# Performance work log

Measured on AMD Instinct MI355X. Metric: run time of the kernel, lower is better.

The kernel has to match this reference:

```python
import jax, jax.numpy as jnp
import numpy as np

H = 16  # num_heads

def setup_inputs() -> dict:
    key = jax.random.key(0)
    ks = jax.random.split(key, 9)
    B, S, D = 4, 1024, 1024
    s = 0.02
    return {
        "x": jax.random.normal(ks[0], (B, S, D), jnp.float32),
        "Wq": jax.random.normal(ks[1], (D, D), jnp.float32) * s,
        "bq": jax.random.normal(ks[2], (D,), jnp.float32) * s,
        "Wk": jax.random.normal(ks[3], (D, D), jnp.float32) * s,
        "bk": jax.random.normal(ks[4], (D,), jnp.float32) * s,
        "Wv": jax.random.normal(ks[5], (D, D), jnp.float32) * s,
        "bv": jax.random.normal(ks[6], (D,), jnp.float32) * s,
        "Wo": jax.random.normal(ks[7], (D, D), jnp.float32) * s,
        "bo": jax.random.normal(ks[8], (D,), jnp.float32) * s,
    }

def reference(x, Wq, bq, Wk, bk, Wv, bv, Wo, bo):
    B, S, D = x.shape
    hd = D // H
    # Batched equivalent of the per-head Linear loop: project then split into heads.
    def proj(W, b):
        return (x @ W + b).reshape(B, S, H, hd).transpose(0, 2, 1, 3)  # [B,H,S,hd]
    q, k, v = proj(Wq, bq), proj(Wk, bk), proj(Wv, bv)
    scores = jnp.einsum("bhqd,bhkd->bhqk", q, k) / jnp.sqrt(jnp.float32(hd))
    probs = jax.nn.softmax(scores, axis=-1)  # [B,H,S,S] (dropout p=0 -> identity)
    ctx = jnp.einsum("bhqk,bhkd->bhqd", probs, v)  # [B,H,S,hd]
    ctx = ctx.transpose(0, 2, 1, 3).reshape(B, S, D)  # concat heads
    out = ctx @ Wo + bo
    return out, probs
```

## Files before the change

kernel.cpp:

```cpp
#include <hip/hip_runtime.h>
#include <math.h>

typedef unsigned short u16;
typedef __attribute__((ext_vector_type(8))) short short8;
typedef __attribute__((ext_vector_type(4))) float f32x4;

#define BB 4
#define SS 1024
#define DD 1024
#define NH 16
#define HD 64
#define BH 64

__device__ __forceinline__ u16 f2bf(float f) {
    union { float f; unsigned u; } v;
    v.f = f;
    unsigned r = v.u + 0x7fffu + ((v.u >> 16) & 1u);
    return (u16)(r >> 16);
}

__device__ __forceinline__ void gll16(const void* g, void* l) {
    __builtin_amdgcn_global_load_lds((__attribute__((address_space(1))) void*)g,
                                     (__attribute__((address_space(3))) void*)l, 16, 0, 0);
}

__global__ void cast_bf16(const float* __restrict__ X, u16* __restrict__ Y) {
    const int i = blockIdx.x * blockDim.x + threadIdx.x;
    const float4 v = reinterpret_cast<const float4*>(X)[i];
    ushort4 o;
    o.x = f2bf(v.x); o.y = f2bf(v.y); o.z = f2bf(v.z); o.w = f2bf(v.w);
    reinterpret_cast<ushort4*>(Y)[i] = o;
}

__global__ void transpose_cast_w(const float* __restrict__ W0, const float* __restrict__ W1,
                                 const float* __restrict__ W2, const float* __restrict__ W3,
                                 u16* __restrict__ O0, u16* __restrict__ O1,
                                 u16* __restrict__ O2, u16* __restrict__ O3) {
    __shared__ float T[64][65];
    const int z = blockIdx.z;
    const float* W = (z == 0) ? W0 : (z == 1) ? W1 : (z == 2) ? W2 : W3;
    u16* O = (z == 0) ? O0 : (z == 1) ? O1 : (z == 2) ? O2 : O3;
    const int k0 = blockIdx.x * 64, n0 = blockIdx.y * 64;
    const int x = threadIdx.x & 63, yq = threadIdx.x >> 6;
#pragma unroll
    for (int r = 0; r < 16; r++) {
        const int row = yq * 16 + r;
        T[row][x] = W[(size_t)(k0 + row) * 1024 + n0 + x];
    }
    __syncthreads();
#pragma unroll
    for (int r = 0; r < 16; r++) {
        const int row = yq * 16 + r;
        O[(size_t)(n0 + row) * 1024 + k0 + x] = f2bf(T[x][row]);
    }
}

__global__ void transpose_v(const u16* __restrict__ V, u16* __restrict__ VT) {
    __shared__ u16 T[64][66];
    const int t0 = blockIdx.x * 64;
    const size_t hbase = (size_t)blockIdx.y * (SS * HD);
    const int x = threadIdx.x & 63, yq = threadIdx.x >> 6;
#pragma unroll
    for (int r = 0; r < 16; r++) {
        const int trow = yq * 16 + r;
        T[trow][x] = V[hbase + (size_t)(t0 + trow) * 64 + x];
    }
    __syncthreads();
#pragma unroll
    for (int r = 0; r < 16; r++) {
        const int drow = yq * 16 + r;
        VT[hbase + (size_t)drow * 1024 + t0 + x] = T[x][drow];
    }
}

template <int MODE, int QKV, int NJC>
__global__ __launch_bounds__(256) void mfma_gemm(
    const u16* __restrict__ A,
    const u16* __restrict__ Bt0, const u16* __restrict__ Bt1, const u16* __restrict__ Bt2,
    const float* __restrict__ bias0, const float* __restrict__ bias1, const float* __restrict__ bias2,
    void* __restrict__ out0, void* __restrict__ out1, void* __restrict__ out2) {
    constexpr int BN = 32 * NJC;
    __shared__ __align__(16) u16 As[128][32];
    __shared__ __align__(16) u16 Bs[BN][32];

    const u16* Bt = Bt0;
    const float* bias = bias0;
    void* out = out0;
    if (QKV) {
        const int z = blockIdx.z;
        Bt = (z == 0) ? Bt0 : (z == 1) ? Bt1 : Bt2;
        bias = (z == 0) ? bias0 : (z == 1) ? bias1 : bias2;
        out = (z == 0) ? out0 : (z == 1) ? out1 : out2;
    }

    const int tid = threadIdx.x;
    const int w = tid >> 6, lane = tid & 63, l15 = lane & 15, quad = lane >> 4;
    const int wr = w >> 1, wc = w & 1;
    const int m0 = blockIdx.y * 128, n0 = blockIdx.x * BN;

    f32x4 acc[4][NJC];
#pragma unroll
    for (int i = 0; i < 4; i++)
#pragma unroll
        for (int j = 0; j < NJC; j++) acc[i][j] = (f32x4){0.f, 0.f, 0.f, 0.f};

    for (int k0 = 0; k0 < 1024; k0 += 32) {
#pragma unroll
        for (int i = 0; i < 2; i++) {
            const int c = i * 256 + tid;
            gll16(A + (size_t)(m0 + (c >> 2)) * 1024 + k0 + (c & 3) * 8,
                  &As[0][0] + (size_t)(i * 256 + (tid & ~63)) * 8);
        }
#pragma unroll
        for (int i = 0; i < BN / 64; i++) {
            const int c = i * 256 + tid;
            gll16(Bt + (size_t)(n0 + (c >> 2)) * 1024 + k0 + (c & 3) * 8,
                  &Bs[0][0] + (size_t)(i * 256 + (tid & ~63)) * 8);
        }
        __syncthreads();
        short8 af[4], bf[NJC];
#pragma unroll
        for (int i = 0; i < 4; i++)
            af[i] = *(const short8*)(&As[wr * 64 + i * 16 + l15][quad * 8]);
#pragma unroll
        for (int j = 0; j < NJC; j++)
            bf[j] = *(const short8*)(&Bs[wc * 16 * NJC + j * 16 + l15][quad * 8]);
#pragma unroll
        for (int i = 0; i < 4; i++)
#pragma unroll
            for (int j = 0; j < NJC; j++)
                acc[i][j] = __builtin_amdgcn_mfma_f32_16x16x32_bf16(af[i], bf[j], acc[i][j], 0, 0, 0);
        __syncthreads();
    }

#pragma unroll
    for (int i = 0; i < 4; i++) {
#pragma unroll
        for (int j = 0; j < NJC; j++) {
            const int nn = n0 + wc * 16 * NJC + j * 16 + l15;
            const float bb = bias[nn];
#pragma unroll
            for (int r = 0; r < 4; r++) {
                const int mm = m0 + wr * 64 + i * 16 + quad * 4 + r;
                const float val = acc[i][j][r] + bb;
                if (MODE == 0) {
                    const int b = mm >> 10, s = mm & 1023, h = nn >> 6, d = nn & 63;
                    ((u16*)out)[((size_t)(b * NH + h) * SS + s) * HD + d] = f2bf(val);
                } else {
                    ((float*)out)[(size_t)mm * 1024 + nn] = val;
                }
            }
        }
    }
}

__global__ __launch_bounds__(256) void attn_fused(
    const u16* __restrict__ Qg, const u16* __restrict__ Kg, const u16* __restrict__ VTg,
    float* __restrict__ probs, u16* __restrict__ ctx) {
    __shared__ __align__(16) u16 Ks[2][2][64][32];
    __shared__ __align__(16) u16 Vs[2][2][64][32];
    __shared__ __align__(16) u16 Ps[4][2][16][32];

    const int tid = threadIdx.x;
    const int w = tid >> 6, lane = tid & 63, l15 = lane & 15, quad = lane >> 4;

    const int bid = blockIdx.y * 16 + blockIdx.x;
    const int work = (bid & 7) * 128 + (bid >> 3);
    const int bh = work >> 4;
    const int s0 = (work & 15) * 64;
    const size_t hbase = (size_t)bh * (SS * HD);

    const int qg = s0 + w * 16 + l15;
    const short8 bq0 = *(const short8*)(Qg + hbase + (size_t)qg * 64 + quad * 8);
    const short8 bq1 = *(const short8*)(Qg + hbase + (size_t)qg * 64 + 32 + quad * 8);

    auto stageK = [&](int buf, int kt) {
#pragma unroll
        for (int i = 0; i < 2; i++) {
            const int c = i * 256 + tid;
            const int ks = c >> 8, row = (c >> 2) & 63, ch = c & 3;
            const int cb = i * 256 + (tid & ~63);
            gll16(Kg + hbase + (size_t)(kt * 64 + row) * 64 + ks * 32 + ch * 8,
                  &Ks[buf][0][0][0] + (size_t)cb * 8);
        }
    };
    auto stageV = [&](int buf, int kt) {
#pragma unroll
        for (int i = 0; i < 2; i++) {
            const int c = i * 256 + tid;
            const int ks = c >> 8, row = (c >> 2) & 63, ch = c & 3;
            const int cb = i * 256 + (tid & ~63);
            gll16(VTg + hbase + (size_t)row * 1024 + kt * 64 + ks * 32 + ch * 8,
                  &Vs[buf][0][0][0] + (size_t)cb * 8);
        }
    };

    float l_i = 0.f;
    stageK(0, 0);
    asm volatile("s_waitcnt vmcnt(0)" ::: "memory");
    __builtin_amdgcn_s_barrier();
#pragma unroll 1
    for (int kt = 0; kt < 16; kt++) {
        const int cur = kt & 1;
        if (kt < 15) stageK(cur ^ 1, kt + 1);
        float ss = 0.f;
#pragma unroll
        for (int c = 0; c < 4; c++) {
            const short8 ak0 = *(const short8*)(&Ks[cur][0][c * 16 + l15][quad * 8]);
            const short8 ak1 = *(const short8*)(&Ks[cur][1][c * 16 + l15][quad * 8]);
            f32x4 z = {0.f, 0.f, 0.f, 0.f};
            z = __builtin_amdgcn_mfma_f32_16x16x32_bf16(ak0, bq0, z, 0, 0, 0);
            z = __builtin_amdgcn_mfma_f32_16x16x32_bf16(ak1, bq1, z, 0, 0, 0);
#pragma unroll
            for (int r = 0; r < 4; r++) ss += __expf(z[r] * 0.125f);
        }
        ss += __shfl_xor(ss, 16);
        ss += __shfl_xor(ss, 32);
        l_i += ss;
        asm volatile("s_waitcnt vmcnt(0)" ::: "memory");
        __builtin_amdgcn_s_barrier();
    }
    const float nlog = -__logf(l_i);

    f32x4 oacc[4];
#pragma unroll
    for (int j = 0; j < 4; j++) oacc[j] = (f32x4){0.f, 0.f, 0.f, 0.f};

    const size_t prow = ((size_t)bh * SS + qg) * SS;

    stageK(0, 0);
    stageV(0, 0);
    asm volatile("s_waitcnt vmcnt(0)" ::: "memory");
    __builtin_amdgcn_s_barrier();

#pragma unroll 1
    for (int kt = 0; kt < 16; kt++) {
        const int cur = kt & 1;
        if (kt < 15) { stageK(cur ^ 1, kt + 1); stageV(cur ^ 1, kt + 1); }

        f32x4 sc[4];
        __builtin_amdgcn_s_setprio(1);
#pragma unroll
        for (int c = 0; c < 4; c++) {
            const short8 ak0 = *(const short8*)(&Ks[cur][0][c * 16 + l15][quad * 8]);
            const short8 ak1 = *(const short8*)(&Ks[cur][1][c * 16 + l15][quad * 8]);
            f32x4 z = {0.f, 0.f, 0.f, 0.f};
            z = __builtin_amdgcn_mfma_f32_16x16x32_bf16(ak0, bq0, z, 0, 0, 0);
            z = __builtin_amdgcn_mfma_f32_16x16x32_bf16(ak1, bq1, z, 0, 0, 0);
            sc[c] = z;
        }
        __builtin_amdgcn_s_setprio(0);
#pragma unroll
        for (int c = 0; c < 4; c++) {
            float p[4];
            f32x4 pv;
#pragma unroll
            for (int r = 0; r < 4; r++) {
                p[r] = __expf(fmaf(sc[c][r], 0.125f, nlog));
                pv[r] = p[r];
            }
            *(f32x4*)(probs + prow + kt * 64 + c * 16 + quad * 4) = pv;
            uint2 pk;
            pk.x = (unsigned)f2bf(p[0]) | ((unsigned)f2bf(p[1]) << 16);
            pk.y = (unsigned)f2bf(p[2]) | ((unsigned)f2bf(p[3]) << 16);
            *(uint2*)(&Ps[w][c >> 1][l15][(c & 1) * 16 + quad * 4]) = pk;
        }
        const short8 ap0 = *(const short8*)(&Ps[w][0][l15][quad * 8]);
        const short8 ap1 = *(const short8*)(&Ps[w][1][l15][quad * 8]);
        __builtin_amdgcn_s_setprio(1);
#pragma unroll
        for (int j = 0; j < 4; j++) {
            const short8 bv0 = *(const short8*)(&Vs[cur][0][j * 16 + l15][quad * 8]);
            const short8 bv1 = *(const short8*)(&Vs[cur][1][j * 16 + l15][quad * 8]);
            oacc[j] = __builtin_amdgcn_mfma_f32_16x16x32_bf16(ap0, bv0, oacc[j], 0, 0, 0);
            oacc[j] = __builtin_amdgcn_mfma_f32_16x16x32_bf16(ap1, bv1, oacc[j], 0, 0, 0);
        }
        __builtin_amdgcn_s_setprio(0);
        asm volatile("s_waitcnt vmcnt(4)" ::: "memory");
        __builtin_amdgcn_s_barrier();
    }

    const int b = bh >> 4, h = bh & 15;
#pragma unroll
    for (int j = 0; j < 4; j++)
#pragma unroll
        for (int r = 0; r < 4; r++) {
            const int s = s0 + w * 16 + quad * 4 + r;
            ctx[((size_t)b * SS + s) * DD + h * HD + j * 16 + l15] = f2bf(oacc[j][r]);
        }
}

extern "C" void kernel_launch(void* const* d_in, const int* in_sizes, int n_in,
                              void* d_out, int out_size, void* d_ws, size_t ws_size,
                              hipStream_t stream) {
    const float* x  = (const float*)d_in[0];
    const float* Wq = (const float*)d_in[1];
    const float* bq = (const float*)d_in[2];
    const float* Wk = (const float*)d_in[3];
    const float* bk = (const float*)d_in[4];
    const float* Wv = (const float*)d_in[5];
    const float* bv = (const float*)d_in[6];
    const float* Wo = (const float*)d_in[7];
    const float* bo = (const float*)d_in[8];

    float* out   = (float*)d_out;
    float* probs = out + (size_t)BB * SS * DD;

    char* ws = (char*)d_ws;
    u16* xb   = (u16*)(ws);
    u16* Wtq  = (u16*)(ws + (8ull << 20));
    u16* Wtk  = (u16*)(ws + (10ull << 20));
    u16* Wtv  = (u16*)(ws + (12ull << 20));
    u16* Wto  = (u16*)(ws + (14ull << 20));
    u16* qb   = (u16*)(ws + (16ull << 20));
    u16* kb   = (u16*)(ws + (24ull << 20));
    u16* vb   = (u16*)(ws + (32ull << 20));
    u16* vTb  = (u16*)(ws + (40ull << 20));
    u16* ctxb = (u16*)(ws + (48ull << 20));

    const dim3 blk(256);

    cast_bf16<<<dim3(4096), blk, 0, stream>>>(x, xb);
    transpose_cast_w<<<dim3(16, 16, 4), blk, 0, stream>>>(Wq, Wk, Wv, Wo, Wtq, Wtk, Wtv, Wto);

    mfma_gemm<0, 1, 4><<<dim3(8, 32, 3), blk, 0, stream>>>(
        xb, Wtq, Wtk, Wtv, bq, bk, bv, qb, kb, vb);

    transpose_v<<<dim3(16, 64), blk, 0, stream>>>(vb, vTb);

    attn_fused<<<dim3(16, 64), blk, 0, stream>>>(qb, kb, vTb, probs, ctxb);

    mfma_gemm<1, 0, 2><<<dim3(16, 32), blk, 0, stream>>>(
        ctxb, Wto, nullptr, nullptr, bo, nullptr, nullptr, out, nullptr, nullptr);
}
```

Measured before the change: 428.6 us.

## Write V transposed from QKV GEMM and double attention block size to 512

The QKV projection GEMM now writes the V output directly in [bh][d][s] transposed layout using 4-wide vector stores, which removes the separate transpose_v kernel and its extra global round trip. The attention kernel moves to 512 threads (8 waves) covering 128 query rows per block, so each staged K/V tile is shared by twice as many query rows and each thread issues one async load per tile instead of two. In exchange, the block uses more LDS and registers, and the grid halves, which may reduce occupancy or load balance.

```diff
diff --git a/kernel.cpp b/kernel.cpp
--- a/kernel.cpp
+++ b/kernel.cpp
@@ -55,24 +55,6 @@
     }
 }
 
-__global__ void transpose_v(const u16* __restrict__ V, u16* __restrict__ VT) {
-    __shared__ u16 T[64][66];
-    const int t0 = blockIdx.x * 64;
-    const size_t hbase = (size_t)blockIdx.y * (SS * HD);
-    const int x = threadIdx.x & 63, yq = threadIdx.x >> 6;
-#pragma unroll
-    for (int r = 0; r < 16; r++) {
-        const int trow = yq * 16 + r;
-        T[trow][x] = V[hbase + (size_t)(t0 + trow) * 64 + x];
-    }
-    __syncthreads();
-#pragma unroll
-    for (int r = 0; r < 16; r++) {
-        const int drow = yq * 16 + r;
-        VT[hbase + (size_t)drow * 1024 + t0 + x] = T[x][drow];
-    }
-}
-
 template <int MODE, int QKV, int NJC>
 __global__ __launch_bounds__(256) void mfma_gemm(
     const u16* __restrict__ A,
@@ -86,11 +68,11 @@
     const u16* Bt = Bt0;
     const float* bias = bias0;
     void* out = out0;
+    const int zz = QKV ? blockIdx.z : 0;
     if (QKV) {
-        const int z = blockIdx.z;
-        Bt = (z == 0) ? Bt0 : (z == 1) ? Bt1 : Bt2;
-        bias = (z == 0) ? bias0 : (z == 1) ? bias1 : bias2;
-        out = (z == 0) ? out0 : (z == 1) ? out1 : out2;
+        Bt = (zz == 0) ? Bt0 : (zz == 1) ? Bt1 : Bt2;
+        bias = (zz == 0) ? bias0 : (zz == 1) ? bias1 : bias2;
+        out = (zz == 0) ? out0 : (zz == 1) ? out1 : out2;
     }
 
     const int tid = threadIdx.x;
@@ -139,35 +121,46 @@
         for (int j = 0; j < NJC; j++) {
             const int nn = n0 + wc * 16 * NJC + j * 16 + l15;
             const float bb = bias[nn];
-#pragma unroll
-            for (int r = 0; r < 4; r++) {
-                const int mm = m0 + wr * 64 + i * 16 + quad * 4 + r;
-                const float val = acc[i][j][r] + bb;
-                if (MODE == 0) {
-                    const int b = mm >> 10, s = mm & 1023, h = nn >> 6, d = nn & 63;
-                    ((u16*)out)[((size_t)(b * NH + h) * SS + s) * HD + d] = f2bf(val);
-                } else {
-                    ((float*)out)[(size_t)mm * 1024 + nn] = val;
+            if (MODE == 0 && QKV && zz == 2) {
+                const int mm0 = m0 + wr * 64 + i * 16 + quad * 4;
+                const int b = mm0 >> 10, s = mm0 & 1023, h = nn >> 6, d = nn & 63;
+                ushort4 o;
+                o.x = f2bf(acc[i][j][0] + bb);
+                o.y = f2bf(acc[i][j][1] + bb);
+                o.z = f2bf(acc[i][j][2] + bb);
+                o.w = f2bf(acc[i][j][3] + bb);
+                *(ushort4*)(&((u16*)out)[((size_t)(b * NH + h) * HD + d) * SS + s]) = o;
+            } else {
+#pragma unroll
+                for (int r = 0; r < 4; r++) {
+                    const int mm = m0 + wr * 64 + i * 16 + quad * 4 + r;
+                    const float val = acc[i][j][r] + bb;
+                    if (MODE == 0) {
+                        const int b = mm >> 10, s = mm & 1023, h = nn >> 6, d = nn & 63;
+                        ((u16*)out)[((size_t)(b * NH + h) * SS + s) * HD + d] = f2bf(val);
+                    } else {
+                        ((float*)out)[(size_t)mm * 1024 + nn] = val;
+                    }
                 }
             }
         }
     }
 }
 
-__global__ __launch_bounds__(256) void attn_fused(
+__global__ __launch_bounds__(512) void attn_fused(
     const u16* __restrict__ Qg, const u16* __restrict__ Kg, const u16* __restrict__ VTg,
     float* __restrict__ probs, u16* __restrict__ ctx) {
     __shared__ __align__(16) u16 Ks[2][2][64][32];
     __shared__ __align__(16) u16 Vs[2][2][64][32];
-    __shared__ __align__(16) u16 Ps[4][2][16][32];
+    __shared__ __align__(16) u16 Ps[8][2][16][32];
 
     const int tid = threadIdx.x;
     const int w = tid >> 6, lane = tid & 63, l15 = lane & 15, quad = lane >> 4;
 
-    const int bid = blockIdx.y * 16 + blockIdx.x;
-    const int work = (bid & 7) * 128 + (bid >> 3);
-    const int bh = work >> 4;
-    const int s0 = (work & 15) * 64;
+    const int bid = blockIdx.y * 8 + blockIdx.x;
+    const int work = (bid & 7) * 64 + (bid >> 3);
+    const int bh = work >> 3;
+    const int s0 = (work & 7) * 128;
     const size_t hbase = (size_t)bh * (SS * HD);
 
     const int qg = s0 + w * 16 + l15;
@@ -175,24 +168,14 @@
     const short8 bq1 = *(const short8*)(Qg + hbase + (size_t)qg * 64 + 32 + quad * 8);
 
     auto stageK = [&](int buf, int kt) {
-#pragma unroll
-        for (int i = 0; i < 2; i++) {
-            const int c = i * 256 + tid;
-            const int ks = c >> 8, row = (c >> 2) & 63, ch = c & 3;
-            const int cb = i * 256 + (tid & ~63);
-            gll16(Kg + hbase + (size_t)(kt * 64 + row) * 64 + ks * 32 + ch * 8,
-                  &Ks[buf][0][0][0] + (size_t)cb * 8);
-        }
+        const int ks = tid >> 8, row = (tid >> 2) & 63, ch = tid & 3;
+        gll16(Kg + hbase + (size_t)(kt * 64 + row) * 64 + ks * 32 + ch * 8,
+              &Ks[buf][0][0][0] + (size_t)(tid & ~63) * 8);
     };
     auto stageV = [&](int buf, int kt) {
-#pragma unroll
-        for (int i = 0; i < 2; i++) {
-            const int c = i * 256 + tid;
-            const int ks = c >> 8, row = (c >> 2) & 63, ch = c & 3;
-            const int cb = i * 256 + (tid & ~63);
-            gll16(VTg + hbase + (size_t)row * 1024 + kt * 64 + ks * 32 + ch * 8,
-                  &Vs[buf][0][0][0] + (size_t)cb * 8);
-        }
+        const int ks = tid >> 8, row = (tid >> 2) & 63, ch = tid & 3;
+        gll16(VTg + hbase + (size_t)row * 1024 + kt * 64 + ks * 32 + ch * 8,
+              &Vs[buf][0][0][0] + (size_t)(tid & ~63) * 8);
     };
 
     float l_i = 0.f;
@@ -314,9 +297,8 @@
     u16* Wto  = (u16*)(ws + (14ull << 20));
     u16* qb   = (u16*)(ws + (16ull << 20));
     u16* kb   = (u16*)(ws + (24ull << 20));
-    u16* vb   = (u16*)(ws + (32ull << 20));
-    u16* vTb  = (u16*)(ws + (40ull << 20));
-    u16* ctxb = (u16*)(ws + (48ull << 20));
+    u16* vTb  = (u16*)(ws + (32ull << 20));
+    u16* ctxb = (u16*)(ws + (40ull << 20));
 
     const dim3 blk(256);
 
@@ -324,11 +306,9 @@
     transpose_cast_w<<<dim3(16, 16, 4), blk, 0, stream>>>(Wq, Wk, Wv, Wo, Wtq, Wtk, Wtv, Wto);
 
     mfma_gemm<0, 1, 4><<<dim3(8, 32, 3), blk, 0, stream>>>(
-        xb, Wtq, Wtk, Wtv, bq, bk, bv, qb, kb, vb);
-
-    transpose_v<<<dim3(16, 64), blk, 0, stream>>>(vb, vTb);
-
-    attn_fused<<<dim3(16, 64), blk, 0, stream>>>(qb, kb, vTb, probs, ctxb);
+        xb, Wtq, Wtk, Wtv, bq, bk, bv, qb, kb, vTb);
+
+    attn_fused<<<dim3(8, 64), dim3(512), 0, stream>>>(qb, kb, vTb, probs, ctxb);
 
     mfma_gemm<1, 0, 2><<<dim3(16, 32), blk, 0, stream>>>(
         ctxb, Wto, nullptr, nullptr, bo, nullptr, nullptr, out, nullptr, nullptr);
```

After: 428.7 us. No clear change (+0.0%).
